# Performance work log

Measured on AMD Instinct MI355X. Metric: run time of the kernel, lower is better.

Reference implementation:

```python
import jax, jax.numpy as jnp
import numpy as np

EPS_CIOU = 1e-7   # keras backend epsilon used inside compute_ciou
EPS = 1e-9        # label-encoder epsilon
ALPHA = 0.5
BETA = 6.0
NUM_CLASSES = 80
TOPK = 10


def compute_ciou(b1, b2):
    """Complete IoU between xyxy boxes b1 (gt) and b2 (pred), broadcastable (...,4)."""
    x1a, y1a, x2a, y2a = b1[..., 0], b1[..., 1], b1[..., 2], b1[..., 3]
    x1b, y1b, x2b, y2b = b2[..., 0], b2[..., 1], b2[..., 2], b2[..., 3]
    w1 = x2a - x1a
    h1 = y2a - y1a + EPS_CIOU
    w2 = x2b - x1b
    h2 = y2b - y1b + EPS_CIOU
    iw = jnp.clip(jnp.minimum(x2a, x2b) - jnp.maximum(x1a, x1b), 0.0, None)
    ih = jnp.clip(jnp.minimum(y2a, y2b) - jnp.maximum(y1a, y1b), 0.0, None)
    inter = iw * ih
    union = w1 * h1 + w2 * h2 - inter
    iou = inter / (union + EPS_CIOU)
    cw = jnp.maximum(x2a, x2b) - jnp.minimum(x1a, x1b)
    ch = jnp.maximum(y2a, y2b) - jnp.minimum(y1a, y1b)
    c2 = cw * cw + ch * ch + EPS_CIOU
    rho2 = ((x1b + x2b - x1a - x2a) ** 2 + (y1b + y2b - y1a - y2a) ** 2) / 4.0
    v = (4.0 / np.pi ** 2) * (jnp.arctan(w2 / h2) - jnp.arctan(w1 / h1)) ** 2
    a = v / (v - iou + (1.0 + EPS_CIOU))
    return iou - (rho2 / c2 + v * a)


def _forward(pd_scores, pd_bboxes, anc_points, gt_labels, gt_bboxes, mask_gt):
    B, A, C = pd_scores.shape
    M = gt_bboxes.shape[1]
    f32 = pd_scores.dtype
    mask_gt_b = mask_gt.astype(bool)                      # (B, M, 1)

    # --- candidate anchors whose center falls inside each gt box ---
    lt = gt_bboxes[:, :, None, :2]                        # (B, M, 1, 2)
    rb = gt_bboxes[:, :, None, 2:]
    anc = anc_points[None, None, :, :]                    # (1, 1, A, 2)
    deltas = jnp.concatenate([anc - lt, rb - anc], -1)    # (B, M, A, 4)
    mask_in_gts = deltas.min(-1) > EPS                    # (B, M, A)
    valid = mask_in_gts & mask_gt_b                       # (B, M, A)

    # --- alignment metric: score^alpha * ciou^beta ---
    ind = gt_labels.astype(jnp.int32)                     # (B, M)
    scores_g = jnp.take_along_axis(pd_scores, jnp.maximum(ind, 0)[:, None, :], axis=-1)  # (B, A, M)
    scores_g = jnp.where(ind[:, None, :] >= 0, scores_g, 0.0)
    scores_g = jnp.transpose(scores_g, (0, 2, 1))         # (B, M, A)
    bbox_scores = jnp.where(valid, scores_g, 0.0)
    iou = compute_ciou(gt_bboxes[:, :, None, :], pd_bboxes[:, None, :, :])  # (B, M, A)
    iou = jnp.maximum(iou, 0.0)
    overlaps = jnp.where(valid, iou, 0.0)
    align_metric = bbox_scores ** ALPHA * overlaps ** BETA

    # --- top-k anchor candidates per gt box ---
    _, topk_idxs = jax.lax.top_k(align_metric, TOPK)      # (B, M, K)
    topk_mask = jnp.broadcast_to(mask_gt_b, (B, M, TOPK))
    topk_idxs = jnp.where(topk_mask, topk_idxs, 0)
    bi = jnp.arange(B)[:, None, None]
    mi = jnp.arange(M)[None, :, None]
    counts = jnp.zeros((B, M, A), f32).at[bi, mi, topk_idxs].add(1.0)
    mask_topk = jnp.where(counts > 1, 0.0, counts)        # duplicates (masked gts) -> 0
    mask_pos = mask_topk * mask_in_gts.astype(f32) * mask_gt.astype(f32)  # (B, M, A)

    # --- break ties: anchor matched to >1 gt keeps highest-IoU gt ---
    fg_mask = mask_pos.sum(axis=1)                        # (B, A)
    mask_multi = jnp.broadcast_to(fg_mask[:, None, :] > 1, (B, M, A))
    is_max = jax.nn.one_hot(jnp.argmax(overlaps, axis=1), M, dtype=f32)  # (B, A, M)
    is_max = jnp.transpose(is_max, (0, 2, 1))             # (B, M, A)
    mask_pos = jnp.where(mask_multi, is_max, mask_pos)
    fg_mask = mask_pos.sum(axis=1)
    target_gt_idx = jnp.argmax(mask_pos, axis=1)          # (B, A)

    # --- gather targets ---
    flat_idx = target_gt_idx + jnp.arange(B, dtype=target_gt_idx.dtype)[:, None] * M
    target_bboxes = gt_bboxes.reshape(-1, 4)[flat_idx]    # (B, A, 4)
    target_labels = jnp.maximum(gt_labels.reshape(-1)[flat_idx], 0.0)
    target_scores = jax.nn.one_hot(target_labels.astype(jnp.int32), C, dtype=f32)  # (B, A, C)
    target_scores = jnp.where((fg_mask > 0)[..., None], target_scores, 0.0)

    # --- normalize class targets by alignment ---
    align_metric = align_metric * mask_pos
    pos_align = align_metric.max(axis=-1, keepdims=True)              # (B, M, 1)
    pos_overlaps = (overlaps * mask_pos).max(axis=-1, keepdims=True)  # (B, M, 1)
    norm = (align_metric * pos_overlaps / (pos_align + EPS)).max(axis=-2)[..., None]  # (B, A, 1)
    target_scores = target_scores * norm

    return (jax.lax.stop_gradient(target_bboxes),
            jax.lax.stop_gradient(target_scores),
            jax.lax.stop_gradient(fg_mask > 0))


def setup_inputs() -> dict:
    key = jax.random.key(0)
    k = jax.random.split(key, 6)
    B, A, C, M = 32, 8400, 80, 64
    IMG = 640.0
    pd_scores = jax.random.uniform(k[0], (B, A, C), jnp.float32)
    pb = jax.random.uniform(k[1], (B, A, 4), jnp.float32) * IMG
    pd_bboxes = jnp.concatenate([jnp.minimum(pb[..., :2], pb[..., 2:]),
                                 jnp.maximum(pb[..., :2], pb[..., 2:])], -1)
    anc_points = jax.random.uniform(k[2], (A, 2), jnp.float32) * IMG
    ctr = jax.random.uniform(k[3], (B, M, 2), jnp.float32) * IMG
    wh = jax.random.uniform(k[4], (B, M, 2), jnp.float32) * 200.0 + 20.0
    gt_bboxes = jnp.concatenate([ctr - wh / 2, ctr + wh / 2], -1)
    gt_labels = jax.random.randint(k[5], (B, M), 0, C).astype(jnp.float32)
    mask_gt = jnp.ones((B, M, 1), jnp.bool_)
    return {"pd_scores": pd_scores, "pd_bboxes": pd_bboxes, "anc_points": anc_points,
            "gt_labels": gt_labels, "gt_bboxes": gt_bboxes, "mask_gt": mask_gt}


def reference(pd_scores, pd_bboxes, anc_points, gt_labels, gt_bboxes, mask_gt):
    return _forward(pd_scores, pd_bboxes, anc_points, gt_labels, gt_bboxes, mask_gt)
```

## Files before the change

### kernel.cpp

```cpp
#include <hip/hip_runtime.h>
#include <cstdint>
#include <cstddef>

#define EPSC 1e-7f
#define EPS9 1e-9f
#define K4PI2 0.40528473456935108577f
#define NTOPK 10
#define SEG 448

__device__ __forceinline__ bool better(float v1, int i1, float v2, int i2) {
    return (v1 > v2) || ((v1 == v2) && (i1 < i2));
}

__device__ __forceinline__ bool mask_at(const unsigned char* mb, int i, int wide) {
    if (wide) return reinterpret_cast<const unsigned int*>(mb)[i] != 0u;
    return mb[i] != 0;
}

__device__ __forceinline__ unsigned long long shfl_xor_u64(unsigned long long v, int off) {
    int lo = __shfl_xor((int)(unsigned)(v & 0xFFFFFFFFull), off);
    int hi = __shfl_xor((int)(unsigned)(v >> 32), off);
    return ((unsigned long long)(unsigned)hi << 32) | (unsigned)lo;
}

__device__ __forceinline__ unsigned lane_rank(unsigned long long ball) {
    return __builtin_amdgcn_mbcnt_hi((unsigned)(ball >> 32),
           __builtin_amdgcn_mbcnt_lo((unsigned)(ball & 0xFFFFFFFFull), 0u));
}

__device__ __forceinline__ int seg_slot(int g, int o1, int o2, int o3) {
    int w = (g >= o1) + (g >= o2) + (g >= o3);
    int off = (w == 0) ? 0 : (w == 1 ? o1 : (w == 2 ? o2 : o3));
    return w * SEG + (g - off);
}

__device__ __forceinline__ float ciou_clip(float x1a, float y1a, float x2a, float y2a,
                                           float w1h1, float atan1,
                                           float4 pb, float at2) {
    float w2 = pb.z - pb.x, h2 = pb.w - pb.y + EPSC;
    float iw = fmaxf(fminf(x2a, pb.z) - fmaxf(x1a, pb.x), 0.f);
    float ih = fmaxf(fminf(y2a, pb.w) - fmaxf(y1a, pb.y), 0.f);
    float inter = iw * ih;
    float uni = w1h1 + w2 * h2 - inter;
    float iou = inter / (uni + EPSC);
    float cw = fmaxf(x2a, pb.z) - fminf(x1a, pb.x);
    float ch = fmaxf(y2a, pb.w) - fminf(y1a, pb.y);
    float c2 = cw * cw + ch * ch + EPSC;
    float dx = pb.x + pb.z - x1a - x2a;
    float dy = pb.y + pb.w - y1a - y2a;
    float rho2 = (dx * dx + dy * dy) * 0.25f;
    float dat = at2 - atan1;
    float vv = K4PI2 * dat * dat;
    float aa = vv / (vv - iou + (1.f + EPSC));
    return fmaxf(iou - (rho2 / c2 + vv * aa), 0.f);
}

__global__ void k_detect(const unsigned char* __restrict__ mask, int n, int* __restrict__ mode) {
    __shared__ int bad;
    if (threadIdx.x == 0) bad = 0;
    __syncthreads();
    const unsigned int* w = reinterpret_cast<const unsigned int*>(mask);
    int nw = n >> 2;
    for (int i = threadIdx.x; i < nw; i += 256) {
        unsigned int v = w[i];
        if (v != 0u && v != 1u && v != 0x3f800000u) atomicOr(&bad, 1);
    }
    __syncthreads();
    if (threadIdx.x == 0) mode[0] = bad ? 0 : 1;
}

__global__ __launch_bounds__(256) void k_topk(
    const float* __restrict__ pd_scores, const float* __restrict__ pd_bboxes,
    const float* __restrict__ anc, const float* __restrict__ gt_labels,
    const float* __restrict__ gt_bboxes, const unsigned char* __restrict__ mask_gt,
    const int* __restrict__ mode,
    int* __restrict__ count, int* __restrict__ win_idx, float* __restrict__ win_al,
    int* __restrict__ win_fl, int* __restrict__ ovf,
    int A, int C, int M, int B)
{
    __shared__ unsigned long long keys[8 * SEG];
    __shared__ int s_cnt[8];
    __shared__ int s_p[2];

    int pbid = blockIdx.x;
    int b = pbid % B;
    int mp = pbid / B;
    int m0 = 2 * mp, m1 = m0 + 1;
    int row0 = b * M + m0, row1 = b * M + m1;
    int tid = threadIdx.x;
    int lane = tid & 63, wid = tid >> 6;
    int wide = mode[0];

    bool v0 = mask_at(mask_gt, row0, wide);
    bool v1 = (m1 < M) && mask_at(mask_gt, row1, wide);
    if (!v0 && !v1) return;

    float x1a0 = 3e38f, y1a0 = 0.f, x2a0 = 0.f, y2a0 = 0.f, w1h10 = 0.f, at10 = 0.f;
    int lbl0 = -1;
    if (v0) {
        float4 g = reinterpret_cast<const float4*>(gt_bboxes)[row0];
        x1a0 = g.x; y1a0 = g.y; x2a0 = g.z; y2a0 = g.w;
        float w1 = x2a0 - x1a0, h1 = y2a0 - y1a0 + EPSC;
        w1h10 = w1 * h1; at10 = atanf(w1 / h1);
        lbl0 = (int)gt_labels[row0];
    }
    float x1a1 = 3e38f, y1a1 = 0.f, x2a1 = 0.f, y2a1 = 0.f, w1h11 = 0.f, at11 = 0.f;
    int lbl1 = -1;
    if (v1) {
        float4 g = reinterpret_cast<const float4*>(gt_bboxes)[row1];
        x1a1 = g.x; y1a1 = g.y; x2a1 = g.z; y2a1 = g.w;
        float w1 = x2a1 - x1a1, h1 = y2a1 - y1a1 + EPSC;
        w1h11 = w1 * h1; at11 = atanf(w1 / h1);
        lbl1 = (int)gt_labels[row1];
    }

    const float4* pb4 = reinterpret_cast<const float4*>(pd_bboxes + (size_t)b * A * 4);
    const float*  ps  = pd_scores + (size_t)b * A * C;
    const float2* an2 = reinterpret_cast<const float2*>(anc);
    const float4* an4 = reinterpret_cast<const float4*>(anc);

    if (tid == 0) { s_p[0] = 0; s_p[1] = 0; }

    int r0 = 0, r1 = 0;
    const int wb0 = wid * SEG, wb1 = (4 + wid) * SEG;
    int aMain = A & ~1023;
#define TEST0(px, py) ((px - x1a0 > EPS9) & (py - y1a0 > EPS9) & (x2a0 - px > EPS9) & (y2a0 - py > EPS9))
#define TEST1(px, py) ((px - x1a1 > EPS9) & (py - y1a1 > EPS9) & (x2a1 - px > EPS9) & (y2a1 - py > EPS9))
#define COMPACT(inb, rr, wb, aa)  { unsigned long long bl = __ballot(inb); \
        int pos = rr + (int)lane_rank(bl); \
        if ((inb) && pos < SEG) keys[wb + pos] = (unsigned long long)(unsigned)(aa); \
        rr += __popcll(bl); }
    for (int base = 0; base < aMain; base += 1024) {
        int a0 = base + (tid << 2);
        int q = a0 >> 1;
        float4 p01 = an4[q];
        float4 p23 = an4[q + 1];
        bool t0, t1;
        t0 = TEST0(p01.x, p01.y); t1 = TEST1(p01.x, p01.y);
        COMPACT(t0, r0, wb0, a0);     COMPACT(t1, r1, wb1, a0);
        t0 = TEST0(p01.z, p01.w); t1 = TEST1(p01.z, p01.w);
        COMPACT(t0, r0, wb0, a0 + 1); COMPACT(t1, r1, wb1, a0 + 1);
        t0 = TEST0(p23.x, p23.y); t1 = TEST1(p23.x, p23.y);
        COMPACT(t0, r0, wb0, a0 + 2); COMPACT(t1, r1, wb1, a0 + 2);
        t0 = TEST0(p23.z, p23.w); t1 = TEST1(p23.z, p23.w);
        COMPACT(t0, r0, wb0, a0 + 3); COMPACT(t1, r1, wb1, a0 + 3);
    }
    for (int a = aMain + tid; a < A; a += 256) {
        float2 ap = an2[a];
        bool t0 = TEST0(ap.x, ap.y), t1 = TEST1(ap.x, ap.y);
        COMPACT(t0, r0, wb0, a);
        COMPACT(t1, r1, wb1, a);
    }
    if (lane == 0) { s_cnt[wid] = r0; s_cnt[4 + wid] = r1; }
    __syncthreads();

    int c00 = s_cnt[0], c01 = s_cnt[1], c02 = s_cnt[2], c03 = s_cnt[3];
    int c10 = s_cnt[4], c11 = s_cnt[5], c12 = s_cnt[6], c13 = s_cnt[7];
    int mx = max(max(max(c00, c01), max(c02, c03)), max(max(c10, c11), max(c12, c13)));
    if (mx > SEG) {
        if (tid == 0) { if (v0) ovf[row0] = 1; if (v1) ovf[row1] = 1; }
        return;
    }
    int o01 = c00, o02 = c00 + c01, o03 = c00 + c01 + c02; int n0 = o03 + c03;
    int o11 = c10, o12 = c10 + c11, o13 = c10 + c11 + c12; int n1 = o13 + c13;
    int nsum = n0 + n1;

    int pc0 = 0, pc1 = 0;
    for (int cidx = tid; cidx < nsum; cidx += 256) {
        bool g1 = cidx >= n0;
        int li = cidx - (g1 ? n0 : 0);
        int slot = (g1 ? 4 * SEG : 0) +
                   seg_slot(li, g1 ? o11 : o01, g1 ? o12 : o02, g1 ? o13 : o03);
        int a = (int)(unsigned)keys[slot];
        float4 pb = pb4[a];
        float x1a = g1 ? x1a1 : x1a0, y1a = g1 ? y1a1 : y1a0;
        float x2a = g1 ? x2a1 : x2a0, y2a = g1 ? y2a1 : y2a0;
        float w1h1 = g1 ? w1h11 : w1h10, at1 = g1 ? at11 : at10;
        int lbl = g1 ? lbl1 : lbl0;
        float w2 = pb.z - pb.x, h2 = pb.w - pb.y + EPSC;
        float at2 = atanf(w2 / h2);
        float ovl = ciou_clip(x1a, y1a, x2a, y2a, w1h1, at1, pb, at2);
        float sc = (lbl >= 0) ? ps[(size_t)a * C + lbl] : 0.f;
        float o2v = ovl * ovl;
        float val = sqrtf(sc) * (o2v * o2v * o2v);
        keys[slot] = ((unsigned long long)__float_as_uint(val) << 32) | (unsigned)(~(unsigned)a);
        bool pos = val > 0.f;
        pc0 += __popcll(__ballot(pos && !g1));
        pc1 += __popcll(__ballot(pos && g1));
    }
    if (lane == 0) { if (pc0) atomicAdd(&s_p[0], pc0); if (pc1) atomicAdd(&s_p[1], pc1); }
    __syncthreads();

    if (wid >= 2) return;
    bool myv = wid ? v1 : v0;
    if (!myv) return;
    int g = wid;
    int gbase = g ? 4 * SEG : 0;
    int ntot = g ? n1 : n0;
    int so1 = g ? o11 : o01, so2 = g ? o12 : o02, so3 = g ? o13 : o03;
    float x1a = g ? x1a1 : x1a0, y1a = g ? y1a1 : y1a0;
    float x2a = g ? x2a1 : x2a0, y2a = g ? y2a1 : y2a0;
    int base_o = (g ? row1 : row0) * NTOPK;
    size_t bA = (size_t)b * A;
    int p = s_p[g];
    int rp = p < NTOPK ? p : NTOPK;

    unsigned long long tv[NTOPK];
#pragma unroll
    for (int j = 0; j < NTOPK; ++j) tv[j] = 0;
    for (int gidx = lane; gidx < ntot; gidx += 64) {
        unsigned long long kk = keys[gbase + seg_slot(gidx, so1, so2, so3)];
        if (kk > tv[NTOPK - 1]) {
            tv[NTOPK - 1] = kk;
#pragma unroll
            for (int j = NTOPK - 1; j > 0; --j)
                if (tv[j] > tv[j - 1]) { unsigned long long t = tv[j]; tv[j] = tv[j - 1]; tv[j - 1] = t; }
        }
    }

    for (int k = 0; k < rp; ++k) {
        unsigned long long head = tv[0];
        unsigned long long best = head;
#pragma unroll
        for (int off = 32; off; off >>= 1) {
            unsigned long long o = shfl_xor_u64(best, off);
            if (o > best) best = o;
        }
        if (head == best && head != 0ull) {
            int a = (int)(~(unsigned)(best & 0xFFFFFFFFull));
            int o = base_o + k;
            win_idx[o] = a;
            win_al[o]  = __uint_as_float((unsigned)(best >> 32));
            win_fl[o]  = 1;
            atomicAdd(&count[bA + a], 1);
#pragma unroll
            for (int j = 0; j < NTOPK - 1; ++j) tv[j] = tv[j + 1];
            tv[NTOPK - 1] = 0;
        }
    }

    if (rp < NTOPK) {
        int iters = (A + 63 - lane) / 64;
        int zp = 0;
        for (int k = rp; k < NTOPK; ++k) {
            unsigned zprop = 0xFFFFFFFFu;
            while (zp < iters) {
                int a = lane + zp * 64;
                float2 ap = an2[a];
                bool in = (ap.x - x1a > EPS9) & (ap.y - y1a > EPS9) &
                          (x2a - ap.x > EPS9) & (y2a - ap.y > EPS9);
                if (!in) { zprop = (unsigned)a; break; }
                ++zp;
            }
            unsigned cprop = 0xFFFFFFFFu;
#pragma unroll
            for (int j = 0; j < NTOPK; ++j) {
                unsigned long long kk = tv[j];
                if (kk != 0ull && kk < (1ull << 32)) {
                    unsigned idx2 = ~(unsigned)kk;
                    if (idx2 < cprop) cprop = idx2;
                }
            }
            unsigned prop = zprop < cprop ? zprop : cprop;
            unsigned bm_ = prop;
#pragma unroll
            for (int off = 32; off; off >>= 1) {
                unsigned o = (unsigned)__shfl_xor((int)bm_, off);
                if (o < bm_) bm_ = o;
            }
            if (bm_ != 0xFFFFFFFFu) {
                if (cprop == bm_ && cprop < zprop) {
                    int o = base_o + k;
                    win_idx[o] = (int)bm_; win_al[o] = 0.f; win_fl[o] = 1;
                    atomicAdd(&count[bA + bm_], 1);
                    unsigned long long wkk = (unsigned long long)(unsigned)(~bm_);
#pragma unroll
                    for (int j = 0; j < NTOPK; ++j) if (tv[j] == wkk) tv[j] = 0;
                } else if (zprop == bm_ && zprop < cprop) {
                    ++zp;
                }
            }
        }
    }
#undef TEST0
#undef TEST1
#undef COMPACT
}

__global__ __launch_bounds__(256) void k_topk_fb(
    const float* __restrict__ pd_scores, const float* __restrict__ pd_bboxes,
    const float* __restrict__ anc, const float* __restrict__ gt_labels,
    const float* __restrict__ gt_bboxes,
    const int* __restrict__ ovf,
    int* __restrict__ count, int* __restrict__ win_idx, float* __restrict__ win_al,
    int* __restrict__ win_fl,
    int A, int C, int M)
{
    int row = blockIdx.x;
    if (!ovf[row]) return;
    int b = row / M;
    int tid = threadIdx.x;

    float4 g = reinterpret_cast<const float4*>(gt_bboxes)[row];
    float x1a = g.x, y1a = g.y, x2a = g.z, y2a = g.w;
    float w1 = x2a - x1a, h1 = y2a - y1a + EPSC;
    float w1h1 = w1 * h1;
    float atan1 = atanf(w1 / h1);
    int lbl = (int)gt_labels[row];

    const float4* pb4 = reinterpret_cast<const float4*>(pd_bboxes + (size_t)b * A * 4);
    const float*  ps  = pd_scores + (size_t)b * A * C;
    const float2* an2 = reinterpret_cast<const float2*>(anc);

    float tv[NTOPK];
    int   ti[NTOPK], tfl[NTOPK];
#pragma unroll
    for (int j = 0; j < NTOPK; ++j) { tv[j] = -1.f; ti[j] = 0x7fffffff; tfl[j] = 0; }

    for (int a = tid; a < A; a += 256) {
        float2 ap = an2[a];
        bool in = (ap.x - x1a > EPS9) & (ap.y - y1a > EPS9) &
                  (x2a - ap.x > EPS9) & (y2a - ap.y > EPS9);
        float val = 0.f;
        if (in) {
            float4 pb = pb4[a];
            float w2 = pb.z - pb.x, h2 = pb.w - pb.y + EPSC;
            float ovl = ciou_clip(x1a, y1a, x2a, y2a, w1h1, atan1, pb, atanf(w2 / h2));
            float sc = (lbl >= 0) ? ps[(size_t)a * C + lbl] : 0.f;
            float o2 = ovl * ovl;
            val = sqrtf(sc) * (o2 * o2 * o2);
        }
        if (better(val, a, tv[NTOPK - 1], ti[NTOPK - 1])) {
            tv[NTOPK - 1] = val; ti[NTOPK - 1] = a; tfl[NTOPK - 1] = in ? 1 : 0;
#pragma unroll
            for (int j = NTOPK - 1; j > 0; --j) {
                if (better(tv[j], ti[j], tv[j - 1], ti[j - 1])) {
                    float fv = tv[j]; tv[j] = tv[j - 1]; tv[j - 1] = fv;
                    int   fi = ti[j]; ti[j] = ti[j - 1]; ti[j - 1] = fi;
                    int   ff = tfl[j]; tfl[j] = tfl[j - 1]; tfl[j - 1] = ff;
                }
            }
        }
    }

    __shared__ float swv[8];
    __shared__ int   swi[8];
    int lane = tid & 63, wid = tid >> 6;
    int base_o = row * NTOPK;

    for (int k = 0; k < NTOPK; ++k) {
        float bv = -2.f; int bi = 0x7fffffff;
#pragma unroll
        for (int j = 0; j < NTOPK; ++j)
            if (better(tv[j], ti[j], bv, bi)) { bv = tv[j]; bi = ti[j]; }
#pragma unroll
        for (int off = 32; off > 0; off >>= 1) {
            float ov = __shfl_xor(bv, off);
            int   oi = __shfl_xor(bi, off);
            if (better(ov, oi, bv, bi)) { bv = ov; bi = oi; }
        }
        if (lane == 0) { swv[wid] = bv; swi[wid] = bi; }
        __syncthreads();
        if (tid == 0) {
            float gv = swv[0]; int gi = swi[0];
            for (int w = 1; w < 4; ++w)
                if (better(swv[w], swi[w], gv, gi)) { gv = swv[w]; gi = swi[w]; }
            swv[7] = gv; swi[7] = gi;
        }
        __syncthreads();
        int gbi = swi[7];
#pragma unroll
        for (int j = 0; j < NTOPK; ++j) {
            if (ti[j] == gbi) {
                int o = base_o + k;
                win_idx[o] = gbi; win_al[o] = tv[j]; win_fl[o] = tfl[j];
                if (tfl[j]) atomicAdd(&count[(size_t)b * A + gbi], 1);
                tv[j] = -2.f; ti[j] = 0x7fffffff;
            }
        }
        __syncthreads();
    }
}

__global__ void k_resolve(
    const float* __restrict__ pd_scores, const float* __restrict__ pd_bboxes,
    const float* __restrict__ anc, const float* __restrict__ gt_labels,
    const float* __restrict__ gt_bboxes, const unsigned char* __restrict__ mask_gt,
    const int* __restrict__ mode,
    const int* __restrict__ count, const int* __restrict__ win_idx,
    const float* __restrict__ win_al, const int* __restrict__ win_fl,
    int* __restrict__ claim_m, float* __restrict__ claim_al,
    float* __restrict__ pos_al, float* __restrict__ pos_ov,
    int A, int C, int M, int total)
{
    int t = blockIdx.x * 256 + threadIdx.x;
    if (t >= total) return;
    int bm = t / NTOPK;
    int b = bm / M, m = bm % M;
    if (!win_fl[t]) return;
    int a = win_idx[t];
    size_t ba = (size_t)b * A + a;
    int cnt = count[ba];
    float al, ov; int mm_out;
    if (cnt == 1) {
        mm_out = m; al = win_al[t];
        float4 gg = reinterpret_cast<const float4*>(gt_bboxes)[b * M + m];
        float w1 = gg.z - gg.x, h1 = gg.w - gg.y + EPSC;
        float4 pb = reinterpret_cast<const float4*>(pd_bboxes)[ba];
        float w2 = pb.z - pb.x, h2p = pb.w - pb.y + EPSC;
        ov = ciou_clip(gg.x, gg.y, gg.z, gg.w, w1 * h1, atanf(w1 / h1), pb, atanf(w2 / h2p));
    } else {
        int wide = mode[0];
        float4 pb = reinterpret_cast<const float4*>(pd_bboxes)[ba];
        float2 ap = reinterpret_cast<const float2*>(anc)[a];
        float w2 = pb.z - pb.x, h2p = pb.w - pb.y + EPSC;
        float at2 = atanf(w2 / h2p);
        float best_ov = -1.f; int best_m = 0, best_valid = 0;
        for (int mm = 0; mm < M; ++mm) {
            float4 gg = reinterpret_cast<const float4*>(gt_bboxes)[b * M + mm];
            bool in = (ap.x - gg.x > EPS9) && (ap.y - gg.y > EPS9) &&
                      (gg.z - ap.x > EPS9) && (gg.w - ap.y > EPS9);
            bool valid = in && mask_at(mask_gt, b * M + mm, wide);
            float ovv = 0.f;
            if (valid) {
                float w1 = gg.z - gg.x, h1 = gg.w - gg.y + EPSC;
                ovv = ciou_clip(gg.x, gg.y, gg.z, gg.w, w1 * h1, atanf(w1 / h1), pb, at2);
            }
            if (ovv > best_ov) { best_ov = ovv; best_m = mm; best_valid = valid ? 1 : 0; }
        }
        int lb = (int)gt_labels[b * M + best_m];
        float sc = (best_valid && lb >= 0) ? pd_scores[ba * C + lb] : 0.f;
        float o2 = best_ov * best_ov;
        mm_out = best_m; al = sqrtf(sc) * (o2 * o2 * o2); ov = best_ov;
    }
    claim_m[ba]  = mm_out;
    claim_al[ba] = al;
    atomicMax((unsigned int*)&pos_al[b * M + mm_out], __float_as_uint(al));
    atomicMax((unsigned int*)&pos_ov[b * M + mm_out], __float_as_uint(ov));
}

__global__ __launch_bounds__(256) void k_final(
    const int* __restrict__ count, const int* __restrict__ claim_m,
    const float* __restrict__ claim_al,
    const float* __restrict__ pos_al, const float* __restrict__ pos_ov,
    const float* __restrict__ gt_labels, const float* __restrict__ gt_bboxes,
    float* __restrict__ out_bb, float* __restrict__ out_ts, float* __restrict__ out_fg,
    int A, int M, int C4, int BA)
{
    __shared__ float s_nv[256];
    __shared__ int   s_lb[256];
    int base_ba = blockIdx.x * 256;
    int tid = threadIdx.x;
    int ba = base_ba + tid;
    if (ba < BA) {
        int b = ba / A;
        int cnt = count[ba];
        int m = claim_m[ba];
        float4 g = reinterpret_cast<const float4*>(gt_bboxes)[b * M + m];
        reinterpret_cast<float4*>(out_bb)[ba] = g;
        float nv = 0.f; int lb = -1;
        if (cnt > 0) {
            lb = max((int)gt_labels[b * M + m], 0);
            nv = claim_al[ba] * pos_ov[b * M + m] / (pos_al[b * M + m] + EPS9);
        }
        out_fg[ba] = (cnt > 0) ? 1.f : 0.f;
        s_nv[tid] = nv; s_lb[tid] = lb;
    } else { s_nv[tid] = 0.f; s_lb[tid] = -1; }
    __syncthreads();
    float4* ts4 = reinterpret_cast<float4*>(out_ts);
    size_t fbase = (size_t)base_ba * C4;
    for (int j = 0; j < C4; ++j) {
        int fl = j * 256 + tid;
        int la = fl / 20;
        int ch;
        if (C4 == 20) { la = fl / 20; ch = fl - la * 20; }
        else          { la = fl / C4; ch = fl - la * C4; }
        int ba2 = base_ba + la;
        if (ba2 < BA) {
            float nv = s_nv[la];
            int lb = s_lb[la];
            int c0 = ch * 4;
            float4 o;
            o.x = (c0     == lb) ? nv : 0.f;
            o.y = (c0 + 1 == lb) ? nv : 0.f;
            o.z = (c0 + 2 == lb) ? nv : 0.f;
            o.w = (c0 + 3 == lb) ? nv : 0.f;
            ts4[fbase + fl] = o;
        }
    }
}

extern "C" void kernel_launch(void* const* d_in, const int* in_sizes, int n_in,
                              void* d_out, int out_size, void* d_ws, size_t ws_size,
                              hipStream_t stream) {
    const float* pd_scores = (const float*)d_in[0];
    const float* pd_bboxes = (const float*)d_in[1];
    const float* anc       = (const float*)d_in[2];
    const float* gt_labels = (const float*)d_in[3];
    const float* gt_bboxes = (const float*)d_in[4];
    const unsigned char* mask_gt = (const unsigned char*)d_in[5];

    int A  = in_sizes[2] / 2;
    int BA = in_sizes[1] / 4;
    int B  = BA / A;
    int C  = in_sizes[0] / BA;
    int M  = in_sizes[3] / B;
    int BM = B * M;

    char* w = (char*)d_ws;
    auto alloc = [&](size_t bytes) { char* p = w; w += ((bytes + 255) / 256) * 256; return p; };
    int*   mode     = (int*)  alloc(256);
    char*  zero_beg = w;
    int*   count    = (int*)  alloc((size_t)BA * 4);
    int*   claim_m  = (int*)  alloc((size_t)BA * 4);
    float* pos_al   = (float*)alloc((size_t)BM * 4);
    float* pos_ov   = (float*)alloc((size_t)BM * 4);
    int*   win_fl   = (int*)  alloc((size_t)BM * NTOPK * 4);
    int*   ovf      = (int*)  alloc((size_t)BM * 4);
    char*  zero_end = w;
    float* claim_al = (float*)alloc((size_t)BA * 4);
    int*   win_idx  = (int*)  alloc((size_t)BM * NTOPK * 4);
    float* win_al   = (float*)alloc((size_t)BM * NTOPK * 4);

    float* out_bb = (float*)d_out;
    float* out_ts = out_bb + (size_t)BA * 4;
    float* out_fg = out_ts + (size_t)BA * C;

    hipMemsetAsync(zero_beg, 0, (size_t)(zero_end - zero_beg), stream);

    k_detect<<<1, 256, 0, stream>>>(mask_gt, BM, mode);
    int nPairs = B * ((M + 1) / 2);
    k_topk<<<nPairs, 256, 0, stream>>>(pd_scores, pd_bboxes, anc, gt_labels, gt_bboxes, mask_gt,
                                       mode, count, win_idx, win_al, win_fl, ovf, A, C, M, B);
    k_topk_fb<<<BM, 256, 0, stream>>>(pd_scores, pd_bboxes, anc, gt_labels, gt_bboxes,
                                      ovf, count, win_idx, win_al, win_fl, A, C, M);
    int nclaims = BM * NTOPK;
    k_resolve<<<(nclaims + 255) / 256, 256, 0, stream>>>(
        pd_scores, pd_bboxes, anc, gt_labels, gt_bboxes, mask_gt, mode,
        count, win_idx, win_al, win_fl, claim_m, claim_al, pos_al, pos_ov, A, C, M, nclaims);
    int C4 = C / 4;
    int gBA = (BA + 255) / 256;
    k_final<<<gBA, 256, 0, stream>>>(count, claim_m, claim_al, pos_al, pos_ov,
                                     gt_labels, gt_bboxes, out_bb, out_ts, out_fg, A, M, C4, BA);
}
```

Baseline: 91.02 us.

## Split top-k into anchor-parallel candidate emission and per-row selection kernels

Replaces the per-gt-pair kernel, which scanned all anchors for two gt boxes, with an anchor-chunk kernel. That kernel tests every anchor against all M gt boxes held in shared memory, computes the CIoU-based alignment only for inside anchors, and appends keys to a global per-row pool through atomics. A second small kernel per gt row then does the top-k selection from that pool. The goal is to avoid rescanning the anchors and recomputing the pred-box atan once per gt pair, and to raise parallelism. In exchange it adds global atomics, workspace pool traffic, an extra launch and a workspace-size-dependent capacity with an overflow fallback.

```diff
diff --git a/kernel.cpp b/kernel.cpp
--- a/kernel.cpp
+++ b/kernel.cpp
@@ -6,7 +6,6 @@
 #define EPS9 1e-9f
 #define K4PI2 0.40528473456935108577f
 #define NTOPK 10
-#define SEG 448
 
 __device__ __forceinline__ bool better(float v1, int i1, float v2, int i2) {
     return (v1 > v2) || ((v1 == v2) && (i1 < i2));
@@ -21,17 +20,6 @@
     int lo = __shfl_xor((int)(unsigned)(v & 0xFFFFFFFFull), off);
     int hi = __shfl_xor((int)(unsigned)(v >> 32), off);
     return ((unsigned long long)(unsigned)hi << 32) | (unsigned)lo;
-}
-
-__device__ __forceinline__ unsigned lane_rank(unsigned long long ball) {
-    return __builtin_amdgcn_mbcnt_hi((unsigned)(ball >> 32),
-           __builtin_amdgcn_mbcnt_lo((unsigned)(ball & 0xFFFFFFFFull), 0u));
-}
-
-__device__ __forceinline__ int seg_slot(int g, int o1, int o2, int o3) {
-    int w = (g >= o1) + (g >= o2) + (g >= o3);
-    int off = (w == 0) ? 0 : (w == 1 ? o1 : (w == 2 ? o2 : o3));
-    return w * SEG + (g - off);
 }
 
 __device__ __forceinline__ float ciou_clip(float x1a, float y1a, float x2a, float y2a,
@@ -69,147 +57,108 @@
     if (threadIdx.x == 0) mode[0] = bad ? 0 : 1;
 }
 
-__global__ __launch_bounds__(256) void k_topk(
+__global__ __launch_bounds__(256) void k_cand(
     const float* __restrict__ pd_scores, const float* __restrict__ pd_bboxes,
     const float* __restrict__ anc, const float* __restrict__ gt_labels,
     const float* __restrict__ gt_bboxes, const unsigned char* __restrict__ mask_gt,
     const int* __restrict__ mode,
-    int* __restrict__ count, int* __restrict__ win_idx, float* __restrict__ win_al,
-    int* __restrict__ win_fl, int* __restrict__ ovf,
-    int A, int C, int M, int B)
+    int* __restrict__ row_cnt, unsigned long long* __restrict__ pool,
+    int* __restrict__ ovf,
+    int A, int C, int M, int B, int CAPROW)
 {
-    __shared__ unsigned long long keys[8 * SEG];
-    __shared__ int s_cnt[8];
-    __shared__ int s_p[2];
-
-    int pbid = blockIdx.x;
-    int b = pbid % B;
-    int mp = pbid / B;
-    int m0 = 2 * mp, m1 = m0 + 1;
-    int row0 = b * M + m0, row1 = b * M + m1;
+    __shared__ float4 s_gt[64];
+    __shared__ float2 s_d[64];
+    __shared__ int    s_l[64];
+
+    int bid = blockIdx.x;
+    int b = bid % B;
+    int chunk = bid / B;
     int tid = threadIdx.x;
-    int lane = tid & 63, wid = tid >> 6;
-    int wide = mode[0];
-
-    bool v0 = mask_at(mask_gt, row0, wide);
-    bool v1 = (m1 < M) && mask_at(mask_gt, row1, wide);
-    if (!v0 && !v1) return;
-
-    float x1a0 = 3e38f, y1a0 = 0.f, x2a0 = 0.f, y2a0 = 0.f, w1h10 = 0.f, at10 = 0.f;
-    int lbl0 = -1;
-    if (v0) {
-        float4 g = reinterpret_cast<const float4*>(gt_bboxes)[row0];
-        x1a0 = g.x; y1a0 = g.y; x2a0 = g.z; y2a0 = g.w;
-        float w1 = x2a0 - x1a0, h1 = y2a0 - y1a0 + EPSC;
-        w1h10 = w1 * h1; at10 = atanf(w1 / h1);
-        lbl0 = (int)gt_labels[row0];
-    }
-    float x1a1 = 3e38f, y1a1 = 0.f, x2a1 = 0.f, y2a1 = 0.f, w1h11 = 0.f, at11 = 0.f;
-    int lbl1 = -1;
-    if (v1) {
-        float4 g = reinterpret_cast<const float4*>(gt_bboxes)[row1];
-        x1a1 = g.x; y1a1 = g.y; x2a1 = g.z; y2a1 = g.w;
-        float w1 = x2a1 - x1a1, h1 = y2a1 - y1a1 + EPSC;
-        w1h11 = w1 * h1; at11 = atanf(w1 / h1);
-        lbl1 = (int)gt_labels[row1];
-    }
-
+
+    if (tid < M) {
+        int row = b * M + tid;
+        bool v = mask_at(mask_gt, row, mode[0]);
+        float4 g;
+        if (v) g = reinterpret_cast<const float4*>(gt_bboxes)[row];
+        else   g = make_float4(3e38f, 3e38f, -3e38f, -3e38f);
+        s_gt[tid] = g;
+        float w1 = g.z - g.x, h1 = g.w - g.y + EPSC;
+        s_d[tid] = make_float2(w1 * h1, atanf(w1 / h1));
+        s_l[tid] = v ? (int)gt_labels[row] : -1;
+    }
+    __syncthreads();
+
+    const float2* an2 = reinterpret_cast<const float2*>(anc);
     const float4* pb4 = reinterpret_cast<const float4*>(pd_bboxes + (size_t)b * A * 4);
     const float*  ps  = pd_scores + (size_t)b * A * C;
-    const float2* an2 = reinterpret_cast<const float2*>(anc);
-    const float4* an4 = reinterpret_cast<const float4*>(anc);
-
-    if (tid == 0) { s_p[0] = 0; s_p[1] = 0; }
-
-    int r0 = 0, r1 = 0;
-    const int wb0 = wid * SEG, wb1 = (4 + wid) * SEG;
-    int aMain = A & ~1023;
-#define TEST0(px, py) ((px - x1a0 > EPS9) & (py - y1a0 > EPS9) & (x2a0 - px > EPS9) & (y2a0 - py > EPS9))
-#define TEST1(px, py) ((px - x1a1 > EPS9) & (py - y1a1 > EPS9) & (x2a1 - px > EPS9) & (y2a1 - py > EPS9))
-#define COMPACT(inb, rr, wb, aa)  { unsigned long long bl = __ballot(inb); \
-        int pos = rr + (int)lane_rank(bl); \
-        if ((inb) && pos < SEG) keys[wb + pos] = (unsigned long long)(unsigned)(aa); \
-        rr += __popcll(bl); }
-    for (int base = 0; base < aMain; base += 1024) {
-        int a0 = base + (tid << 2);
-        int q = a0 >> 1;
-        float4 p01 = an4[q];
-        float4 p23 = an4[q + 1];
-        bool t0, t1;
-        t0 = TEST0(p01.x, p01.y); t1 = TEST1(p01.x, p01.y);
-        COMPACT(t0, r0, wb0, a0);     COMPACT(t1, r1, wb1, a0);
-        t0 = TEST0(p01.z, p01.w); t1 = TEST1(p01.z, p01.w);
-        COMPACT(t0, r0, wb0, a0 + 1); COMPACT(t1, r1, wb1, a0 + 1);
-        t0 = TEST0(p23.x, p23.y); t1 = TEST1(p23.x, p23.y);
-        COMPACT(t0, r0, wb0, a0 + 2); COMPACT(t1, r1, wb1, a0 + 2);
-        t0 = TEST0(p23.z, p23.w); t1 = TEST1(p23.z, p23.w);
-        COMPACT(t0, r0, wb0, a0 + 3); COMPACT(t1, r1, wb1, a0 + 3);
-    }
-    for (int a = aMain + tid; a < A; a += 256) {
-        float2 ap = an2[a];
-        bool t0 = TEST0(ap.x, ap.y), t1 = TEST1(ap.x, ap.y);
-        COMPACT(t0, r0, wb0, a);
-        COMPACT(t1, r1, wb1, a);
-    }
-    if (lane == 0) { s_cnt[wid] = r0; s_cnt[4 + wid] = r1; }
-    __syncthreads();
-
-    int c00 = s_cnt[0], c01 = s_cnt[1], c02 = s_cnt[2], c03 = s_cnt[3];
-    int c10 = s_cnt[4], c11 = s_cnt[5], c12 = s_cnt[6], c13 = s_cnt[7];
-    int mx = max(max(max(c00, c01), max(c02, c03)), max(max(c10, c11), max(c12, c13)));
-    if (mx > SEG) {
-        if (tid == 0) { if (v0) ovf[row0] = 1; if (v1) ovf[row1] = 1; }
-        return;
-    }
-    int o01 = c00, o02 = c00 + c01, o03 = c00 + c01 + c02; int n0 = o03 + c03;
-    int o11 = c10, o12 = c10 + c11, o13 = c10 + c11 + c12; int n1 = o13 + c13;
-    int nsum = n0 + n1;
-
-    int pc0 = 0, pc1 = 0;
-    for (int cidx = tid; cidx < nsum; cidx += 256) {
-        bool g1 = cidx >= n0;
-        int li = cidx - (g1 ? n0 : 0);
-        int slot = (g1 ? 4 * SEG : 0) +
-                   seg_slot(li, g1 ? o11 : o01, g1 ? o12 : o02, g1 ? o13 : o03);
-        int a = (int)(unsigned)keys[slot];
-        float4 pb = pb4[a];
-        float x1a = g1 ? x1a1 : x1a0, y1a = g1 ? y1a1 : y1a0;
-        float x2a = g1 ? x2a1 : x2a0, y2a = g1 ? y2a1 : y2a0;
-        float w1h1 = g1 ? w1h11 : w1h10, at1 = g1 ? at11 : at10;
-        int lbl = g1 ? lbl1 : lbl0;
-        float w2 = pb.z - pb.x, h2 = pb.w - pb.y + EPSC;
-        float at2 = atanf(w2 / h2);
-        float ovl = ciou_clip(x1a, y1a, x2a, y2a, w1h1, at1, pb, at2);
-        float sc = (lbl >= 0) ? ps[(size_t)a * C + lbl] : 0.f;
-        float o2v = ovl * ovl;
-        float val = sqrtf(sc) * (o2v * o2v * o2v);
-        keys[slot] = ((unsigned long long)__float_as_uint(val) << 32) | (unsigned)(~(unsigned)a);
-        bool pos = val > 0.f;
-        pc0 += __popcll(__ballot(pos && !g1));
-        pc1 += __popcll(__ballot(pos && g1));
-    }
-    if (lane == 0) { if (pc0) atomicAdd(&s_p[0], pc0); if (pc1) atomicAdd(&s_p[1], pc1); }
-    __syncthreads();
-
-    if (wid >= 2) return;
-    bool myv = wid ? v1 : v0;
-    if (!myv) return;
-    int g = wid;
-    int gbase = g ? 4 * SEG : 0;
-    int ntot = g ? n1 : n0;
-    int so1 = g ? o11 : o01, so2 = g ? o12 : o02, so3 = g ? o13 : o03;
-    float x1a = g ? x1a1 : x1a0, y1a = g ? y1a1 : y1a0;
-    float x2a = g ? x2a1 : x2a0, y2a = g ? y2a1 : y2a0;
-    int base_o = (g ? row1 : row0) * NTOPK;
+
+    int a0 = chunk * 512 + tid;
+    int a1 = a0 + 256;
+    bool okA = a0 < A, okB = a1 < A;
+    float2 apA = okA ? an2[a0] : make_float2(0.f, 0.f);
+    float2 apB = okB ? an2[a1] : make_float2(0.f, 0.f);
+    float4 pbA = okA ? pb4[a0] : make_float4(0.f, 0.f, 0.f, 0.f);
+    float4 pbB = okB ? pb4[a1] : make_float4(0.f, 0.f, 0.f, 0.f);
+    float atA = okA ? atanf((pbA.z - pbA.x) / (pbA.w - pbA.y + EPSC)) : 0.f;
+    float atB = okB ? atanf((pbB.z - pbB.x) / (pbB.w - pbB.y + EPSC)) : 0.f;
+
+    unsigned long long mk0 = 0, mk1 = 0;
+    for (int m = 0; m < M; ++m) {
+        float4 g = s_gt[m];
+        bool iA = okA & (apA.x - g.x > EPS9) & (apA.y - g.y > EPS9) &
+                        (g.z - apA.x > EPS9) & (g.w - apA.y > EPS9);
+        bool iB = okB & (apB.x - g.x > EPS9) & (apB.y - g.y > EPS9) &
+                        (g.z - apB.x > EPS9) & (g.w - apB.y > EPS9);
+        mk0 |= (unsigned long long)iA << m;
+        mk1 |= (unsigned long long)iB << m;
+    }
+
+    auto emit = [&](int m, int a, const float4& pb, float at2) {
+        int row = b * M + m;
+        int slot = atomicAdd(&row_cnt[row], 1);
+        if (slot < CAPROW) {
+            float4 g = s_gt[m]; float2 d = s_d[m]; int lbl = s_l[m];
+            float ovl = ciou_clip(g.x, g.y, g.z, g.w, d.x, d.y, pb, at2);
+            float sc = (lbl >= 0) ? ps[(size_t)a * C + lbl] : 0.f;
+            float o2 = ovl * ovl;
+            float val = sqrtf(sc) * (o2 * o2 * o2);
+            pool[(size_t)row * CAPROW + slot] =
+                ((unsigned long long)__float_as_uint(val) << 32) | (unsigned)(~(unsigned)a);
+        } else {
+            ovf[row] = 1;
+        }
+    };
+    while (mk0) { int m = __builtin_ctzll(mk0); mk0 &= mk0 - 1; emit(m, a0, pbA, atA); }
+    while (mk1) { int m = __builtin_ctzll(mk1); mk1 &= mk1 - 1; emit(m, a1, pbB, atB); }
+}
+
+__global__ __launch_bounds__(64) void k_sel(
+    const unsigned long long* __restrict__ pool, const int* __restrict__ row_cnt,
+    const int* __restrict__ ovf, const unsigned char* __restrict__ mask_gt,
+    const int* __restrict__ mode,
+    const float* __restrict__ gt_bboxes, const float* __restrict__ anc,
+    int* __restrict__ count, int* __restrict__ win_idx, float* __restrict__ win_al,
+    int* __restrict__ win_fl,
+    int A, int M, int CAPROW)
+{
+    int row = blockIdx.x;
+    if (ovf[row]) return;
+    if (!mask_at(mask_gt, row, mode[0])) return;
+    int lane = threadIdx.x;
+    int cnt = row_cnt[row];
+    if (cnt > CAPROW) return;
+    int b = row / M;
     size_t bA = (size_t)b * A;
-    int p = s_p[g];
-    int rp = p < NTOPK ? p : NTOPK;
-
+    int base_o = row * NTOPK;
+
+    const unsigned long long* rp = pool + (size_t)row * CAPROW;
     unsigned long long tv[NTOPK];
 #pragma unroll
     for (int j = 0; j < NTOPK; ++j) tv[j] = 0;
-    for (int gidx = lane; gidx < ntot; gidx += 64) {
-        unsigned long long kk = keys[gbase + seg_slot(gidx, so1, so2, so3)];
+    int pcnt = 0;
+    for (int i = lane; i < cnt; i += 64) {
+        unsigned long long kk = rp[i];
+        pcnt += (kk >> 32) ? 1 : 0;
         if (kk > tv[NTOPK - 1]) {
             tv[NTOPK - 1] = kk;
 #pragma unroll
@@ -217,8 +166,12 @@
                 if (tv[j] > tv[j - 1]) { unsigned long long t = tv[j]; tv[j] = tv[j - 1]; tv[j - 1] = t; }
         }
     }
-
-    for (int k = 0; k < rp; ++k) {
+#pragma unroll
+    for (int off = 32; off; off >>= 1) pcnt += __shfl_xor(pcnt, off);
+    int p = pcnt;
+    int rpos = p < NTOPK ? p : NTOPK;
+
+    for (int k = 0; k < rpos; ++k) {
         unsigned long long head = tv[0];
         unsigned long long best = head;
 #pragma unroll
@@ -239,10 +192,13 @@
         }
     }
 
-    if (rp < NTOPK) {
+    if (rpos < NTOPK) {
+        float4 g = reinterpret_cast<const float4*>(gt_bboxes)[row];
+        float x1a = g.x, y1a = g.y, x2a = g.z, y2a = g.w;
+        const float2* an2 = reinterpret_cast<const float2*>(anc);
         int iters = (A + 63 - lane) / 64;
         int zp = 0;
-        for (int k = rp; k < NTOPK; ++k) {
+        for (int k = rpos; k < NTOPK; ++k) {
             unsigned zprop = 0xFFFFFFFFu;
             while (zp < iters) {
                 int a = lane + zp * 64;
@@ -282,15 +238,13 @@
             }
         }
     }
-#undef TEST0
-#undef TEST1
-#undef COMPACT
 }
 
 __global__ __launch_bounds__(256) void k_topk_fb(
     const float* __restrict__ pd_scores, const float* __restrict__ pd_bboxes,
     const float* __restrict__ anc, const float* __restrict__ gt_labels,
-    const float* __restrict__ gt_bboxes,
+    const float* __restrict__ gt_bboxes, const unsigned char* __restrict__ mask_gt,
+    const int* __restrict__ mode,
     const int* __restrict__ ovf,
     int* __restrict__ count, int* __restrict__ win_idx, float* __restrict__ win_al,
     int* __restrict__ win_fl,
@@ -298,6 +252,7 @@
 {
     int row = blockIdx.x;
     if (!ovf[row]) return;
+    if (!mask_at(mask_gt, row, mode[0])) return;
     int b = row / M;
     int tid = threadIdx.x;
 
@@ -471,10 +426,8 @@
     size_t fbase = (size_t)base_ba * C4;
     for (int j = 0; j < C4; ++j) {
         int fl = j * 256 + tid;
-        int la = fl / 20;
-        int ch;
-        if (C4 == 20) { la = fl / 20; ch = fl - la * 20; }
-        else          { la = fl / C4; ch = fl - la * C4; }
+        int la = fl / C4;
+        int ch = fl - la * C4;
         int ba2 = base_ba + la;
         if (ba2 < BA) {
             float nv = s_nv[la];
@@ -517,10 +470,16 @@
     float* pos_ov   = (float*)alloc((size_t)BM * 4);
     int*   win_fl   = (int*)  alloc((size_t)BM * NTOPK * 4);
     int*   ovf      = (int*)  alloc((size_t)BM * 4);
+    int*   row_cnt  = (int*)  alloc((size_t)BM * 4);
     char*  zero_end = w;
     float* claim_al = (float*)alloc((size_t)BA * 4);
     int*   win_idx  = (int*)  alloc((size_t)BM * NTOPK * 4);
     float* win_al   = (float*)alloc((size_t)BM * NTOPK * 4);
+    size_t used = (size_t)(w - (char*)d_ws);
+    size_t avail = (ws_size > used + 256) ? (ws_size - used - 256) : 0;
+    long long caprow_ll = (long long)(avail / ((size_t)BM * 8));
+    int CAPROW = caprow_ll > 1536 ? 1536 : (int)caprow_ll;
+    unsigned long long* pool = (unsigned long long*)alloc((size_t)BM * (CAPROW > 0 ? CAPROW : 0) * 8);
 
     float* out_bb = (float*)d_out;
     float* out_ts = out_bb + (size_t)BA * 4;
@@ -529,11 +488,19 @@
     hipMemsetAsync(zero_beg, 0, (size_t)(zero_end - zero_beg), stream);
 
     k_detect<<<1, 256, 0, stream>>>(mask_gt, BM, mode);
-    int nPairs = B * ((M + 1) / 2);
-    k_topk<<<nPairs, 256, 0, stream>>>(pd_scores, pd_bboxes, anc, gt_labels, gt_bboxes, mask_gt,
-                                       mode, count, win_idx, win_al, win_fl, ovf, A, C, M, B);
+
+    bool fast = (M <= 64) && (CAPROW >= 64);
+    if (fast) {
+        int CH = (A + 511) / 512;
+        k_cand<<<B * CH, 256, 0, stream>>>(pd_scores, pd_bboxes, anc, gt_labels, gt_bboxes,
+                                           mask_gt, mode, row_cnt, pool, ovf, A, C, M, B, CAPROW);
+        k_sel<<<BM, 64, 0, stream>>>(pool, row_cnt, ovf, mask_gt, mode, gt_bboxes, anc,
+                                     count, win_idx, win_al, win_fl, A, M, CAPROW);
+    } else {
+        hipMemsetAsync(ovf, 1, (size_t)BM * 4, stream);
+    }
     k_topk_fb<<<BM, 256, 0, stream>>>(pd_scores, pd_bboxes, anc, gt_labels, gt_bboxes,
-                                      ovf, count, win_idx, win_al, win_fl, A, C, M);
+                                      mask_gt, mode, ovf, count, win_idx, win_al, win_fl, A, C, M);
     int nclaims = BM * NTOPK;
     k_resolve<<<(nclaims + 255) / 256, 256, 0, stream>>>(
         pd_scores, pd_bboxes, anc, gt_labels, gt_bboxes, mask_gt, mode,
```

Measured after the change: 173.8 us. 91.0% more time.
